# Performance work log

Measured on AMD Instinct MI355X. Metric: run time of the kernel, lower is better.

## Reference

```python
import jax, jax.numpy as jnp
import numpy as np

D_MODEL = 1024
N_HEADS = 16
FEA = 512
BATCH = 16
D_FF = 2048
HALF = D_MODEL // 2  # d_model / 2**fd_num with fd_num=1
INV_SQRT2 = 1.0 / np.sqrt(2.0).astype(np.float32)


def conv1d_circ(x, w, b):
    # x: (B, C_in, L); w: (C_out, C_in, 3); circular padding of 1 each side
    xp = jnp.pad(x, ((0, 0), (0, 0), (1, 1)), mode='wrap')
    y = jax.lax.conv_general_dilated(xp, w, (1,), 'VALID',
                                     dimension_numbers=('NCH', 'OIH', 'NCH'))
    return y + b[None, :, None]


def layer_norm(x, g, b):
    m = jnp.mean(x, axis=-1, keepdims=True)
    v = jnp.mean((x - m) ** 2, axis=-1, keepdims=True)
    return (x - m) / jnp.sqrt(v + 1e-5) * g + b


def setup_inputs() -> dict:
    key = jax.random.key(0)
    ks = jax.random.split(key, 16)
    s = 0.02
    inp = {
        'x': jax.random.normal(ks[0], (BATCH, FEA, D_MODEL), dtype=jnp.float32),
        'Wq': jax.random.normal(ks[1], (D_MODEL, HALF, 3), dtype=jnp.float32) * s,
        'bq': jnp.zeros((D_MODEL,), jnp.float32),
        'Wk': jax.random.normal(ks[2], (D_MODEL, HALF, 3), dtype=jnp.float32) * s,
        'bk': jnp.zeros((D_MODEL,), jnp.float32),
        'Wv': jax.random.normal(ks[3], (D_MODEL, HALF, 3), dtype=jnp.float32) * s,
        'bv': jnp.zeros((D_MODEL,), jnp.float32),
        'uns_w': jax.random.normal(ks[4], (FEA, 2 * FEA, 3), dtype=jnp.float32) * s,
        'uns_b': jnp.zeros((FEA,), jnp.float32),
        'cv_w1': jax.random.normal(ks[5], (D_FF, D_MODEL, 3), dtype=jnp.float32) * s,
        'cv_b1': jnp.zeros((D_FF,), jnp.float32),
        'cv_w2': jax.random.normal(ks[6], (HALF, D_FF, 3), dtype=jnp.float32) * s,
        'cv_b2': jnp.zeros((HALF,), jnp.float32),
        'cv_g': jnp.ones((HALF,), jnp.float32),
        'cv_beta': jnp.zeros((HALF,), jnp.float32),
        'up_w1': jax.random.normal(ks[7], (D_FF, HALF, 3), dtype=jnp.float32) * s,
        'up_b1': jnp.zeros((D_FF,), jnp.float32),
        'up_w2': jax.random.normal(ks[8], (D_MODEL, D_FF, 3), dtype=jnp.float32) * s,
        'up_b2': jnp.zeros((D_MODEL,), jnp.float32),
        'up_g': jnp.ones((D_MODEL,), jnp.float32),
        'up_beta': jnp.zeros((D_MODEL,), jnp.float32),
    }
    return inp


def reference(x, Wq, bq, Wk, bk, Wv, bv, uns_w, uns_b,
              cv_w1, cv_b1, cv_w2, cv_b2, cv_g, cv_beta,
              up_w1, up_b1, up_w2, up_b2, up_g, up_beta):
    x_input = x
    # torch code detaches x before the wavelet transform -> no grad through this branch
    xd = jax.lax.stop_gradient(x)
    # Haar (db1) single-level DWT along last axis (even length -> exact pairwise)
    x1 = (xd[..., 0::2] + xd[..., 1::2]) * INV_SQRT2  # cA: (B, F, HALF)
    x2 = (xd[..., 0::2] - xd[..., 1::2]) * INV_SQRT2  # cD: (B, F, HALF)

    def proj(z, w, b):  # (B, F, HALF) -> (B, F, D_MODEL)
        return conv1d_circ(z.swapaxes(1, 2), w, b).swapaxes(1, 2)

    def heads(z):  # (B, F, D_MODEL) -> (B, H, F, dh)
        b_, f_, _ = z.shape
        return z.reshape(b_, f_, N_HEADS, -1).transpose(0, 2, 1, 3)

    qh, kh, vh = heads(proj(x1, Wq, bq)), heads(proj(x1, Wk, bk)), heads(proj(x1, Wv, bv))
    ql, kl, vl = heads(proj(x2, Wq, bq)), heads(proj(x2, Wk, bk)), heads(proj(x2, Wv, bv))

    scale = 1.0 / np.sqrt(N_HEADS).astype(np.float32)  # note: module scales by sqrt(n_heads)
    b_, f_ = x.shape[0], x.shape[1]

    hp = jax.nn.softmax(jnp.einsum('bhqd,bhkd->bhqk', qh, kl) * scale, axis=-1)
    h_ctx = jnp.einsum('bhqk,bhkd->bhqd', hp, vh).transpose(0, 2, 1, 3).reshape(b_, f_, -1)
    lp = jax.nn.softmax(jnp.einsum('bhqd,bhkd->bhqk', ql, kh) * scale, axis=-1)
    l_ctx = jnp.einsum('bhqk,bhkd->bhqd', lp, vl).transpose(0, 2, 1, 3).reshape(b_, f_, -1)

    ctx = jnp.concatenate([h_ctx, l_ctx], axis=1)          # (B, 2F, D_MODEL)
    ctx = conv1d_circ(ctx, uns_w, uns_b)                    # channels=2F -> F, length=D_MODEL

    # Convlayer: conv over fea axis, channels D_MODEL -> D_FF -> HALF, then LN
    h = conv1d_circ(ctx.swapaxes(1, 2), cv_w1, cv_b1)
    h = conv1d_circ(jax.nn.relu(h), cv_w2, cv_b2)
    ctx = layer_norm(h.swapaxes(1, 2), cv_g, cv_beta)       # (B, F, HALF)

    # upsizeConvlayer: HALF -> D_FF -> D_MODEL, then LN
    h = conv1d_circ(ctx.swapaxes(1, 2), up_w1, up_b1)
    h = conv1d_circ(jax.nn.relu(h), up_w2, up_b2)
    out = layer_norm(h.swapaxes(1, 2), up_g, up_beta)       # (B, F, D_MODEL)
    return out + x_input
```

## Files before the change

### kernel.cpp

```cpp
#include <hip/hip_runtime.h>
#include <hip/hip_bf16.h>

#define B_    16
#define FEA_  512
#define DM_   1024
#define HALF_ 512
#define DFF_  2048

typedef unsigned short u16;
typedef __attribute__((ext_vector_type(8))) short bf16x8;
typedef __attribute__((ext_vector_type(4))) float f32x4;

__device__ __forceinline__ float bf2f(u16 u) {
  union { unsigned int i; float f; } v; v.i = ((unsigned int)u) << 16; return v.f;
}
__device__ __forceinline__ u16 f2bf(float f) {
  union { float f; unsigned int i; } v; v.f = f;
  unsigned int x = v.i;
  return (u16)((x + 0x7fffu + ((x >> 16) & 1u)) >> 16);
}
__device__ __forceinline__ void gload16(const u16* g, u16* l) {
  __builtin_amdgcn_global_load_lds(
      (const __attribute__((address_space(1))) void*)g,
      (__attribute__((address_space(3))) void*)l, 16, 0, 0);
}

__global__ void dwt_kernel(const float* __restrict__ x, u16* __restrict__ x1,
                           u16* __restrict__ x2, int n) {
  int i = blockIdx.x * 256 + threadIdx.x;
  if (i >= n) return;
  float2 v = ((const float2*)x)[i];
  x1[i] = f2bf((v.x + v.y) * 0.70710678118f);
  x2[i] = f2bf((v.x - v.y) * 0.70710678118f);
}

__global__ void wtrans_kernel(const float* __restrict__ w, u16* __restrict__ wt,
                              int Cout, int Cin) {
  int e = blockIdx.x * 256 + threadIdx.x;
  if (e >= Cout * Cin * 3) return;
  int co = e / (Cin * 3);
  int r  = e - co * Cin * 3;
  int ci = r / 3;
  int t  = r - ci * 3;
  wt[((size_t)t * Cout + co) * Cin + ci] = f2bf(w[e]);
}

#define ZS_GLOAD(c0_)                                                        \
  {                                                                          \
    _Pragma("unroll") for (int i_ = 0; i_ < 5; ++i_) {                       \
      int e_ = tid + i_ * 256;                                               \
      if (e_ < 130 * 8) {                                                    \
        int r_ = e_ >> 3, c_ = e_ & 7;                                       \
        int gl_ = l0 + r_ - 1;                                               \
        if (gl_ < 0) gl_ += L; else if (gl_ >= L) gl_ -= L;                  \
        gload16(Zb + (size_t)gl_ * Cin + (c0_) + ((c_ ^ (r_ & 7)) * 8),      \
                smem + ((size_t)(i_ * 256 + (tid & 192)) * 8));              \
      }                                                                      \
    }                                                                        \
  }
#define WS_ISSUE(t_, c0_, buf_)                                              \
  {                                                                          \
    const u16* Wg_ = Wt + ((size_t)(t_) * Cout + co0) * Cin + (c0_);         \
    int c_ = lane & 7;                                                       \
    _Pragma("unroll") for (int i_ = 0; i_ < 4; ++i_) {                       \
      int rw_ = (i_ * 4 + w) * 8 + (lane >> 3);                              \
      gload16(Wg_ + (size_t)rw_ * Cin + ((c_ ^ (rw_ & 7)) * 8),              \
              &Wb[(buf_)][(i_ * 4 + w) * 8][0]);                             \
    }                                                                        \
  }

__global__ __launch_bounds__(256, 2) void conv_mfma_kernel(
    const u16* __restrict__ Z, const u16* __restrict__ Wt,
    const float* __restrict__ bias, u16* __restrict__ out,
    int L, int Cin, int Cout, int osl, int osc, int relu) {
  __shared__ __align__(16) u16 smem[130 * 64 + 3 * 128 * 64];
  u16 (*Zs)[64] = (u16(*)[64])smem;
  u16 (*Wb)[128][64] = (u16(*)[128][64])(smem + 130 * 64);
  int l0 = blockIdx.x * 128, co0 = blockIdx.y * 128, b = blockIdx.z;
  int tid = threadIdx.x;
  int lane = tid & 63, w = tid >> 6, wr = w >> 1, wc = w & 1;
  int row16 = lane & 15, g4 = lane >> 4;
  f32x4 acc[4][4];
#pragma unroll
  for (int i = 0; i < 4; ++i)
#pragma unroll
    for (int j = 0; j < 4; ++j) acc[i][j] = (f32x4){0.f, 0.f, 0.f, 0.f};
  const u16* Zb = Z + (size_t)b * L * Cin;

  int nchunk = (Cin >> 6) * 3;
  ZS_GLOAD(0);
  WS_ISSUE(0, 0, 0);
  WS_ISSUE(1, 0, 1);

  for (int k = 0; k < nchunk; ++k) {
    int t = k % 3;
    int c0 = (k / 3) << 6;
    int cur = k % 3;
    if (k + 1 < nchunk) asm volatile("s_waitcnt vmcnt(4)" ::: "memory");
    else                asm volatile("s_waitcnt vmcnt(0)" ::: "memory");
    __builtin_amdgcn_s_barrier();
#pragma unroll
    for (int ks = 0; ks < 2; ++ks) {
      int s = ks * 4 + g4;
      bf16x8 af[4], bfr[4];
#pragma unroll
      for (int mi = 0; mi < 4; ++mi) {
        int ra = wr * 64 + mi * 16 + row16 + t;
        af[mi] = *(const bf16x8*)&Zs[ra][(s ^ (ra & 7)) * 8];
      }
#pragma unroll
      for (int ni = 0; ni < 4; ++ni) {
        int rb = wc * 64 + ni * 16 + row16;
        bfr[ni] = *(const bf16x8*)&Wb[cur][rb][(s ^ (rb & 7)) * 8];
      }
#pragma unroll
      for (int mi = 0; mi < 4; ++mi)
#pragma unroll
        for (int ni = 0; ni < 4; ++ni)
          acc[mi][ni] = __builtin_amdgcn_mfma_f32_16x16x32_bf16(
              af[mi], bfr[ni], acc[mi][ni], 0, 0, 0);
    }
    if ((t == 2) && (c0 + 64 < Cin)) {
      __builtin_amdgcn_s_barrier();
      ZS_GLOAD(c0 + 64);
    }
    if (k + 2 < nchunk) WS_ISSUE((k + 2) % 3, ((k + 2) / 3) << 6, (k + 2) % 3);
  }

  __syncthreads();
  const int TP = 136;
  u16* tile = smem;
  size_t ob = (size_t)b * L * Cout;
  int S, rowbase, colbase;
  if (osc == 1) { S = osl; rowbase = l0; colbase = co0; }
  else          { S = osc; rowbase = co0; colbase = l0; }
#pragma unroll
  for (int ni = 0; ni < 4; ++ni) {
    int c_loc = wc * 64 + ni * 16 + row16;
    float bz = bias[co0 + c_loc];
#pragma unroll
    for (int mi = 0; mi < 4; ++mi) {
#pragma unroll
      for (int r = 0; r < 4; ++r) {
        int l_loc = wr * 64 + mi * 16 + g4 * 4 + r;
        float v = acc[mi][ni][r] + bz;
        if (relu) v = fmaxf(v, 0.f);
        int row = (osc == 1) ? l_loc : c_loc;
        int col = (osc == 1) ? c_loc : l_loc;
        tile[row * TP + col] = f2bf(v);
      }
    }
  }
  __syncthreads();
  for (int e = tid; e < 128 * 16; e += 256) {
    int row = e >> 4, c8 = (e & 15) * 8;
    *(uint4*)(out + ob + (size_t)(rowbase + row) * S + colbase + c8) =
        *(const uint4*)&tile[row * TP + c8];
  }
}

__global__ __launch_bounds__(256, 4) void attn_mfma_kernel(
    const u16* __restrict__ qh, const u16* __restrict__ kh, const u16* __restrict__ vhT,
    const u16* __restrict__ ql, const u16* __restrict__ kl, const u16* __restrict__ vlT,
    u16* __restrict__ ctx) {
  __shared__ u16 Qs[64][72], Ks[64][72], Vts[64][72];
  __shared__ u16 Ps[64][72];
  __shared__ float rsl[2][2][32];
  int qt = blockIdx.x, h = blockIdx.y, bz = blockIdx.z;
  int b = bz >> 1, br = bz & 1;
  const u16* Q  = br ? ql  : qh;
  const u16* K  = br ? kh  : kl;
  const u16* Vt = br ? vlT : vhT;
  int tid = threadIdx.x;
  int lane = tid & 63, w = tid >> 6, wr = w >> 1, wc = w & 1;
  int row16 = lane & 15, g4 = lane >> 4, k8 = g4 * 8;
  int q0 = qt * 64;
  size_t baseQK = (size_t)b * FEA_ * DM_ + h * 64;
  size_t baseV  = (size_t)b * DM_ * FEA_ + (size_t)(h * 64) * FEA_;
  for (int e = tid; e < 64 * 8; e += 256) {
    int r = e >> 3, c = e & 7;
    *(uint4*)&Qs[r][c * 8] = *(const uint4*)(Q + baseQK + (size_t)(q0 + r) * DM_ + c * 8);
  }
  f32x4 oacc[2][2];
  float rsum[2][4];
#pragma unroll
  for (int i = 0; i < 2; ++i) {
#pragma unroll
    for (int j = 0; j < 2; ++j) oacc[i][j] = (f32x4){0.f, 0.f, 0.f, 0.f};
#pragma unroll
    for (int r = 0; r < 4; ++r) rsum[i][r] = 0.f;
  }
  for (int kt = 0; kt < 8; ++kt) {
    __syncthreads();
    for (int e = tid; e < 64 * 8; e += 256) {
      int r = e >> 3, c = e & 7;
      *(uint4*)&Ks[r][c * 8]  = *(const uint4*)(K + baseQK + (size_t)(kt * 64 + r) * DM_ + c * 8);
      *(uint4*)&Vts[r][c * 8] = *(const uint4*)(Vt + baseV + (size_t)r * FEA_ + kt * 64 + c * 8);
    }
    __syncthreads();
    f32x4 sacc[2][2];
#pragma unroll
    for (int i = 0; i < 2; ++i)
#pragma unroll
      for (int j = 0; j < 2; ++j) sacc[i][j] = (f32x4){0.f, 0.f, 0.f, 0.f};
#pragma unroll
    for (int ks = 0; ks < 2; ++ks) {
      int k0 = ks * 32 + k8;
      bf16x8 a0 = *(const bf16x8*)&Qs[wr * 32 + row16][k0];
      bf16x8 a1 = *(const bf16x8*)&Qs[wr * 32 + 16 + row16][k0];
      bf16x8 b0 = *(const bf16x8*)&Ks[wc * 32 + row16][k0];
      bf16x8 b1 = *(const bf16x8*)&Ks[wc * 32 + 16 + row16][k0];
      sacc[0][0] = __builtin_amdgcn_mfma_f32_16x16x32_bf16(a0, b0, sacc[0][0], 0, 0, 0);
      sacc[0][1] = __builtin_amdgcn_mfma_f32_16x16x32_bf16(a0, b1, sacc[0][1], 0, 0, 0);
      sacc[1][0] = __builtin_amdgcn_mfma_f32_16x16x32_bf16(a1, b0, sacc[1][0], 0, 0, 0);
      sacc[1][1] = __builtin_amdgcn_mfma_f32_16x16x32_bf16(a1, b1, sacc[1][1], 0, 0, 0);
    }
#pragma unroll
    for (int mi = 0; mi < 2; ++mi)
#pragma unroll
      for (int ni = 0; ni < 2; ++ni)
#pragma unroll
        for (int r = 0; r < 4; ++r) {
          float p = __expf(sacc[mi][ni][r] * 0.25f);
          rsum[mi][r] += p;
          Ps[wr * 32 + mi * 16 + g4 * 4 + r][wc * 32 + ni * 16 + row16] = f2bf(p);
        }
    __syncthreads();
#pragma unroll
    for (int ks = 0; ks < 2; ++ks) {
      int k0 = ks * 32 + k8;
      bf16x8 a0 = *(const bf16x8*)&Ps[wr * 32 + row16][k0];
      bf16x8 a1 = *(const bf16x8*)&Ps[wr * 32 + 16 + row16][k0];
      bf16x8 b0 = *(const bf16x8*)&Vts[wc * 32 + row16][k0];
      bf16x8 b1 = *(const bf16x8*)&Vts[wc * 32 + 16 + row16][k0];
      oacc[0][0] = __builtin_amdgcn_mfma_f32_16x16x32_bf16(a0, b0, oacc[0][0], 0, 0, 0);
      oacc[0][1] = __builtin_amdgcn_mfma_f32_16x16x32_bf16(a0, b1, oacc[0][1], 0, 0, 0);
      oacc[1][0] = __builtin_amdgcn_mfma_f32_16x16x32_bf16(a1, b0, oacc[1][0], 0, 0, 0);
      oacc[1][1] = __builtin_amdgcn_mfma_f32_16x16x32_bf16(a1, b1, oacc[1][1], 0, 0, 0);
    }
  }
#pragma unroll
  for (int mi = 0; mi < 2; ++mi)
#pragma unroll
    for (int r = 0; r < 4; ++r) {
#pragma unroll
      for (int m = 1; m < 16; m <<= 1) rsum[mi][r] += __shfl_xor(rsum[mi][r], m);
    }
  if (row16 == 0) {
#pragma unroll
    for (int mi = 0; mi < 2; ++mi)
#pragma unroll
      for (int r = 0; r < 4; ++r) rsl[wr][wc][mi * 16 + g4 * 4 + r] = rsum[mi][r];
  }
  __syncthreads();
#pragma unroll
  for (int mi = 0; mi < 2; ++mi)
#pragma unroll
    for (int ni = 0; ni < 2; ++ni)
#pragma unroll
      for (int r = 0; r < 4; ++r) {
        int qq = mi * 16 + g4 * 4 + r;
        float denom = rsl[wr][0][qq] + rsl[wr][1][qq];
        float o = oacc[mi][ni][r] / denom;
        Ps[wc * 32 + ni * 16 + row16][wr * 32 + qq] = f2bf(o);
      }
  __syncthreads();
  for (int e = tid; e < 64 * 8; e += 256) {
    int r = e >> 3, c = e & 7;
    size_t dst = ((size_t)b * DM_ + h * 64 + r) * (2 * FEA_) + br * 512 + q0 + c * 8;
    *(uint4*)(ctx + dst) = *(const uint4*)&Ps[r][c * 8];
  }
}

template <int RESID>
__global__ void ln_kernel(const u16* __restrict__ in, const float* __restrict__ g,
                          const float* __restrict__ beta, const float* __restrict__ resid,
                          void* __restrict__ outp, int C) {
  int row = blockIdx.x;
  int tid = threadIdx.x;
  const u16* p = in + (size_t)row * C;
  float s = 0.f, ss = 0.f;
  for (int c = tid; c < C; c += 256) {
    float v = bf2f(p[c]);
    s += v; ss += v * v;
  }
#pragma unroll
  for (int m = 1; m < 64; m <<= 1) { s += __shfl_xor(s, m); ss += __shfl_xor(ss, m); }
  __shared__ float red[2][4];
  int wid = tid >> 6, lane = tid & 63;
  if (lane == 0) { red[0][wid] = s; red[1][wid] = ss; }
  __syncthreads();
  s  = red[0][0] + red[0][1] + red[0][2] + red[0][3];
  ss = red[1][0] + red[1][1] + red[1][2] + red[1][3];
  float m  = s / C;
  float var = ss / C - m * m;
  float inv = rsqrtf(var + 1e-5f);
  for (int c = tid; c < C; c += 256) {
    float v = (bf2f(p[c]) - m) * inv * g[c] + beta[c];
    if (RESID) ((float*)outp)[(size_t)row * C + c] = v + resid[(size_t)row * C + c];
    else       ((u16*)outp)[(size_t)row * C + c]   = f2bf(v);
  }
}

extern "C" void kernel_launch(void* const* d_in, const int* in_sizes, int n_in,
                              void* d_out, int out_size, void* d_ws, size_t ws_size,
                              hipStream_t stream) {
  (void)in_sizes; (void)n_in; (void)out_size; (void)ws_size;
  const float* x      = (const float*)d_in[0];
  const float* Wq     = (const float*)d_in[1];
  const float* bq     = (const float*)d_in[2];
  const float* Wk     = (const float*)d_in[3];
  const float* bk     = (const float*)d_in[4];
  const float* Wv     = (const float*)d_in[5];
  const float* bv     = (const float*)d_in[6];
  const float* uns_w  = (const float*)d_in[7];
  const float* uns_b  = (const float*)d_in[8];
  const float* cv_w1  = (const float*)d_in[9];
  const float* cv_b1  = (const float*)d_in[10];
  const float* cv_w2  = (const float*)d_in[11];
  const float* cv_b2  = (const float*)d_in[12];
  const float* cv_g   = (const float*)d_in[13];
  const float* cv_beta= (const float*)d_in[14];
  const float* up_w1  = (const float*)d_in[15];
  const float* up_b1  = (const float*)d_in[16];
  const float* up_w2  = (const float*)d_in[17];
  const float* up_b2  = (const float*)d_in[18];
  const float* up_g   = (const float*)d_in[19];
  const float* up_beta= (const float*)d_in[20];

  char* ws = (char*)d_ws;
  const size_t MB = 1ull << 20;
  u16* x1    = (u16*)(ws + 0);
  u16* x2    = (u16*)(ws + 8 * MB);
  u16* qhb   = (u16*)(ws + 16 * MB);
  u16* khb   = (u16*)(ws + 32 * MB);
  u16* vhb   = (u16*)(ws + 48 * MB);
  u16* qlb   = (u16*)(ws + 64 * MB);
  u16* klb   = (u16*)(ws + 80 * MB);
  u16* vlb   = (u16*)(ws + 96 * MB);
  u16* wt_proj = (u16*)d_out;
  u16* ctx   = (u16*)d_out;
  u16* wt_uns = (u16*)(ws + 0);
  u16* ctx2  = (u16*)(ws + 16 * MB);
  u16* wt_cv1 = (u16*)(ws + 32 * MB);
  u16* h1    = (u16*)(ws + 56 * MB);
  u16* wt_cv2 = (u16*)(ws + 32 * MB);
  u16* h2    = (u16*)(ws + 0);
  u16* ctx3  = (u16*)(ws + 8 * MB);
  u16* wt_up1 = (u16*)(ws + 16 * MB);
  u16* h3    = (u16*)(ws + 32 * MB);
  u16* wt_up2 = (u16*)(ws + 64 * MB);
  u16* h4    = (u16*)(ws + 16 * MB);

  dwt_kernel<<<(B_ * FEA_ * HALF_ + 255) / 256, 256, 0, stream>>>(x, x1, x2, B_ * FEA_ * HALF_);

  auto wtr = [&](const float* w, u16* wt, int Cout, int Cin) {
    wtrans_kernel<<<(Cout * Cin * 3 + 255) / 256, 256, 0, stream>>>(w, wt, Cout, Cin);
  };
  auto conv = [&](const u16* Z, const u16* wt, const float* bias, u16* out, int L,
                  int Cin, int Cout, int osl, int osc, int relu) {
    conv_mfma_kernel<<<dim3(L / 128, Cout / 128, B_), 256, 0, stream>>>(
        Z, wt, bias, out, L, Cin, Cout, osl, osc, relu);
  };

  wtr(Wq, wt_proj, DM_, HALF_);
  conv(x1, wt_proj, bq, qhb, FEA_, HALF_, DM_, DM_, 1, 0);
  conv(x2, wt_proj, bq, qlb, FEA_, HALF_, DM_, DM_, 1, 0);
  wtr(Wk, wt_proj, DM_, HALF_);
  conv(x1, wt_proj, bk, khb, FEA_, HALF_, DM_, DM_, 1, 0);
  conv(x2, wt_proj, bk, klb, FEA_, HALF_, DM_, DM_, 1, 0);
  wtr(Wv, wt_proj, DM_, HALF_);
  conv(x1, wt_proj, bv, vhb, FEA_, HALF_, DM_, 1, FEA_, 0);
  conv(x2, wt_proj, bv, vlb, FEA_, HALF_, DM_, 1, FEA_, 0);

  attn_mfma_kernel<<<dim3(8, 16, 32), 256, 0, stream>>>(qhb, khb, vhb, qlb, klb, vlb, ctx);

  wtr(uns_w, wt_uns, FEA_, 2 * FEA_);
  conv(ctx, wt_uns, uns_b, ctx2, DM_, 2 * FEA_, FEA_, 1, DM_, 0);

  wtr(cv_w1, wt_cv1, DFF_, DM_);
  conv(ctx2, wt_cv1, cv_b1, h1, FEA_, DM_, DFF_, DFF_, 1, 1);
  wtr(cv_w2, wt_cv2, HALF_, DFF_);
  conv(h1, wt_cv2, cv_b2, h2, FEA_, DFF_, HALF_, HALF_, 1, 0);
  ln_kernel<0><<<B_ * FEA_, 256, 0, stream>>>(h2, cv_g, cv_beta, nullptr, ctx3, HALF_);

  wtr(up_w1, wt_up1, DFF_, HALF_);
  conv(ctx3, wt_up1, up_b1, h3, FEA_, HALF_, DFF_, DFF_, 1, 1);
  wtr(up_w2, wt_up2, DM_, DFF_);
  conv(h3, wt_up2, up_b2, h4, FEA_, DFF_, DM_, DM_, 1, 0);
  ln_kernel<1><<<B_ * FEA_, 256, 0, stream>>>(h4, up_g, up_beta, x, d_out, DM_);
}
```

Baseline: 748.6 us.

## Batch weight transposes and merge high/low projection convs into larger launches

All three projection weights are transposed in one kernel, and the five later conv weights are transposed in a second single kernel. The x1/x2 projections now run as one conv launch with grid z=32, relying on contiguous workspace placement of x1/x2 and of the high/low outputs. This cuts the launch count from many small kernels to a few larger ones. MFMA blocks are also wrapped in s_setprio to raise wave priority during matrix math. The workspace layout is reshuffled to avoid aliasing, which risks correctness if buffers overlap.

```diff
diff --git a/kernel.cpp b/kernel.cpp
--- a/kernel.cpp
+++ b/kernel.cpp
@@ -34,15 +34,39 @@
   x2[i] = f2bf((v.x - v.y) * 0.70710678118f);
 }
 
-__global__ void wtrans_kernel(const float* __restrict__ w, u16* __restrict__ wt,
-                              int Cout, int Cin) {
+__global__ void wtrans3_kernel(const float* __restrict__ w0, const float* __restrict__ w1,
+                               const float* __restrict__ w2, u16* __restrict__ wt,
+                               int Cout, int Cin) {
+  int n = Cout * Cin * 3;
   int e = blockIdx.x * 256 + threadIdx.x;
-  if (e >= Cout * Cin * 3) return;
-  int co = e / (Cin * 3);
-  int r  = e - co * Cin * 3;
+  if (e >= 3 * n) return;
+  int i = e / n, le = e - i * n;
+  const float* w = (i == 0) ? w0 : ((i == 1) ? w1 : w2);
+  int co = le / (Cin * 3);
+  int r  = le - co * Cin * 3;
   int ci = r / 3;
   int t  = r - ci * 3;
-  wt[((size_t)t * Cout + co) * Cin + ci] = f2bf(w[e]);
+  wt[(size_t)i * n + ((size_t)t * Cout + co) * Cin + ci] = f2bf(w[le]);
+}
+
+struct WTSeg { const float* src; u16* dst; int cout, cin, base; };
+struct WT5 { WTSeg s[5]; int total; };
+__global__ void wtrans5_kernel(WT5 p) {
+  int e = blockIdx.x * 256 + threadIdx.x;
+  if (e >= p.total) return;
+#pragma unroll
+  for (int i = 0; i < 5; ++i) {
+    int Cin = p.s[i].cin, Cout = p.s[i].cout;
+    int n = Cout * Cin * 3;
+    int le = e - p.s[i].base;
+    if (le >= 0 && le < n) {
+      int co = le / (Cin * 3);
+      int r  = le - co * Cin * 3;
+      int ci = r / 3;
+      int t  = r - ci * 3;
+      p.s[i].dst[((size_t)t * Cout + co) * Cin + ci] = f2bf(p.s[i].src[le]);
+    }
+  }
 }
 
 #define ZS_GLOAD(c0_)                                                        \
@@ -113,12 +137,14 @@
         int rb = wc * 64 + ni * 16 + row16;
         bfr[ni] = *(const bf16x8*)&Wb[cur][rb][(s ^ (rb & 7)) * 8];
       }
+      __builtin_amdgcn_s_setprio(1);
 #pragma unroll
       for (int mi = 0; mi < 4; ++mi)
 #pragma unroll
         for (int ni = 0; ni < 4; ++ni)
           acc[mi][ni] = __builtin_amdgcn_mfma_f32_16x16x32_bf16(
               af[mi], bfr[ni], acc[mi][ni], 0, 0, 0);
+      __builtin_amdgcn_s_setprio(0);
     }
     if ((t == 2) && (c0 + 64 < Cin)) {
       __builtin_amdgcn_s_barrier();
@@ -331,62 +357,66 @@
   char* ws = (char*)d_ws;
   const size_t MB = 1ull << 20;
   u16* x1    = (u16*)(ws + 0);
-  u16* x2    = (u16*)(ws + 8 * MB);
+  u16* x1x2  = x1;
   u16* qhb   = (u16*)(ws + 16 * MB);
-  u16* khb   = (u16*)(ws + 32 * MB);
-  u16* vhb   = (u16*)(ws + 48 * MB);
-  u16* qlb   = (u16*)(ws + 64 * MB);
-  u16* klb   = (u16*)(ws + 80 * MB);
+  u16* khb   = (u16*)(ws + 48 * MB);
+  u16* vhb   = (u16*)(ws + 80 * MB);
+  u16* qlb   = (u16*)(ws + 32 * MB);
+  u16* klb   = (u16*)(ws + 64 * MB);
   u16* vlb   = (u16*)(ws + 96 * MB);
   u16* wt_proj = (u16*)d_out;
   u16* ctx   = (u16*)d_out;
-  u16* wt_uns = (u16*)(ws + 0);
-  u16* ctx2  = (u16*)(ws + 16 * MB);
-  u16* wt_cv1 = (u16*)(ws + 32 * MB);
-  u16* h1    = (u16*)(ws + 56 * MB);
-  u16* wt_cv2 = (u16*)(ws + 32 * MB);
-  u16* h2    = (u16*)(ws + 0);
-  u16* ctx3  = (u16*)(ws + 8 * MB);
-  u16* wt_up1 = (u16*)(ws + 16 * MB);
-  u16* h3    = (u16*)(ws + 32 * MB);
-  u16* wt_up2 = (u16*)(ws + 64 * MB);
-  u16* h4    = (u16*)(ws + 16 * MB);
-
-  dwt_kernel<<<(B_ * FEA_ * HALF_ + 255) / 256, 256, 0, stream>>>(x, x1, x2, B_ * FEA_ * HALF_);
-
-  auto wtr = [&](const float* w, u16* wt, int Cout, int Cin) {
-    wtrans_kernel<<<(Cout * Cin * 3 + 255) / 256, 256, 0, stream>>>(w, wt, Cout, Cin);
-  };
+  u16* wt_uns  = (u16*)(ws + 0);
+  u16* wt_cv1  = (u16*)(ws + 4 * MB);
+  u16* wt_cv2  = (u16*)(ws + 17 * MB);
+  u16* wt_up1  = (u16*)(ws + 24 * MB);
+  u16* wt_up2  = (u16*)(ws + 31 * MB);
+  u16* ctx2  = (u16*)(ws + 48 * MB);
+  u16* h1    = (u16*)(ws + 64 * MB);
+  u16* h2    = (u16*)(ws + 96 * MB);
+  u16* ctx3  = (u16*)(ws + 104 * MB);
+  u16* h3    = (u16*)(ws + 64 * MB);
+  u16* h4    = (u16*)(ws + 48 * MB);
+
+  dwt_kernel<<<(B_ * FEA_ * HALF_ + 255) / 256, 256, 0, stream>>>(x, x1, (u16*)(ws + 8 * MB),
+                                                                  B_ * FEA_ * HALF_);
+
+  const int NPROJ = DM_ * HALF_ * 3;
+  wtrans3_kernel<<<(3 * NPROJ + 255) / 256, 256, 0, stream>>>(Wq, Wk, Wv, wt_proj, DM_, HALF_);
+
   auto conv = [&](const u16* Z, const u16* wt, const float* bias, u16* out, int L,
-                  int Cin, int Cout, int osl, int osc, int relu) {
-    conv_mfma_kernel<<<dim3(L / 128, Cout / 128, B_), 256, 0, stream>>>(
+                  int Cin, int Cout, int osl, int osc, int relu, int nb) {
+    conv_mfma_kernel<<<dim3(L / 128, Cout / 128, nb), 256, 0, stream>>>(
         Z, wt, bias, out, L, Cin, Cout, osl, osc, relu);
   };
 
-  wtr(Wq, wt_proj, DM_, HALF_);
-  conv(x1, wt_proj, bq, qhb, FEA_, HALF_, DM_, DM_, 1, 0);
-  conv(x2, wt_proj, bq, qlb, FEA_, HALF_, DM_, DM_, 1, 0);
-  wtr(Wk, wt_proj, DM_, HALF_);
-  conv(x1, wt_proj, bk, khb, FEA_, HALF_, DM_, DM_, 1, 0);
-  conv(x2, wt_proj, bk, klb, FEA_, HALF_, DM_, DM_, 1, 0);
-  wtr(Wv, wt_proj, DM_, HALF_);
-  conv(x1, wt_proj, bv, vhb, FEA_, HALF_, DM_, 1, FEA_, 0);
-  conv(x2, wt_proj, bv, vlb, FEA_, HALF_, DM_, 1, FEA_, 0);
+  conv(x1x2, wt_proj,              bq, qhb, FEA_, HALF_, DM_, DM_, 1, 0, 32);
+  conv(x1x2, wt_proj + NPROJ,      bk, khb, FEA_, HALF_, DM_, DM_, 1, 0, 32);
+  conv(x1x2, wt_proj + 2 * NPROJ,  bv, vhb, FEA_, HALF_, DM_, 1, FEA_, 0, 32);
 
   attn_mfma_kernel<<<dim3(8, 16, 32), 256, 0, stream>>>(qhb, khb, vhb, qlb, klb, vlb, ctx);
 
-  wtr(uns_w, wt_uns, FEA_, 2 * FEA_);
-  conv(ctx, wt_uns, uns_b, ctx2, DM_, 2 * FEA_, FEA_, 1, DM_, 0);
-
-  wtr(cv_w1, wt_cv1, DFF_, DM_);
-  conv(ctx2, wt_cv1, cv_b1, h1, FEA_, DM_, DFF_, DFF_, 1, 1);
-  wtr(cv_w2, wt_cv2, HALF_, DFF_);
-  conv(h1, wt_cv2, cv_b2, h2, FEA_, DFF_, HALF_, HALF_, 1, 0);
+  WT5 p;
+  int base = 0;
+  auto seg = [&](int i, const float* src, u16* dst, int cout, int cin) {
+    p.s[i] = {src, dst, cout, cin, base};
+    base += cout * cin * 3;
+  };
+  seg(0, uns_w, wt_uns, FEA_, 2 * FEA_);
+  seg(1, cv_w1, wt_cv1, DFF_, DM_);
+  seg(2, cv_w2, wt_cv2, HALF_, DFF_);
+  seg(3, up_w1, wt_up1, DFF_, HALF_);
+  seg(4, up_w2, wt_up2, DM_, DFF_);
+  p.total = base;
+  wtrans5_kernel<<<(p.total + 255) / 256, 256, 0, stream>>>(p);
+
+  conv(ctx, wt_uns, uns_b, ctx2, DM_, 2 * FEA_, FEA_, 1, DM_, 0, B_);
+
+  conv(ctx2, wt_cv1, cv_b1, h1, FEA_, DM_, DFF_, DFF_, 1, 1, B_);
+  conv(h1, wt_cv2, cv_b2, h2, FEA_, DFF_, HALF_, HALF_, 1, 0, B_);
   ln_kernel<0><<<B_ * FEA_, 256, 0, stream>>>(h2, cv_g, cv_beta, nullptr, ctx3, HALF_);
 
-  wtr(up_w1, wt_up1, DFF_, HALF_);
-  conv(ctx3, wt_up1, up_b1, h3, FEA_, HALF_, DFF_, DFF_, 1, 1);
-  wtr(up_w2, wt_up2, DM_, DFF_);
-  conv(h3, wt_up2, up_b2, h4, FEA_, DFF_, DM_, DM_, 1, 0);
+  conv(ctx3, wt_up1, up_b1, h3, FEA_, HALF_, DFF_, DFF_, 1, 1, B_);
+  conv(h3, wt_up2, up_b2, h4, FEA_, DFF_, DM_, DM_, 1, 0, B_);
   ln_kernel<1><<<B_ * FEA_, 256, 0, stream>>>(h4, up_g, up_beta, x, d_out, DM_);
 }
```

Result: faster. 713.0 us (-4.7%).
